# Optimization experiments

Hardware: AMD Instinct MI355X
Metric: run time of the kernel (lower is better)

## Reference

```python
import jax, jax.numpy as jnp
import numpy as np

N_NODES = 100000


def gcn_conv(x, edge_index, W, b):
    """PyG-style GCNConv: symmetric-normalized A+I propagation of x @ W, plus bias."""
    n = x.shape[0]
    src, dst = edge_index[0], edge_index[1]
    loops = jnp.arange(n, dtype=src.dtype)
    src = jnp.concatenate([src, loops])  # add self loops
    dst = jnp.concatenate([dst, loops])
    deg = jax.ops.segment_sum(jnp.ones_like(src, dtype=x.dtype), dst, num_segments=n)
    dinv = jnp.where(deg > 0, jax.lax.rsqrt(deg), 0.0)
    norm = dinv[src] * dinv[dst]  # [E+n]
    h = x @ W  # [n, out]
    msg = h[src] * norm[:, None]  # gather + scale
    out = jax.ops.segment_sum(msg, dst, num_segments=n)  # scatter-add
    return out + b


def setup_inputs() -> dict:
    key = jax.random.key(0)
    ks = jax.random.split(key, 5)
    x = jax.random.normal(ks[0], (N_NODES, 4), dtype=jnp.float32)
    edge_index = jax.random.randint(ks[1], (2, 3200000), 0, N_NODES, dtype=jnp.int64)
    W1 = jax.random.normal(ks[2], (4, 64), dtype=jnp.float32) * 0.5
    b1 = jnp.zeros((64,), dtype=jnp.float32)
    W2 = jax.random.normal(ks[3], (64, 32), dtype=jnp.float32) * 0.125
    b2 = jnp.zeros((32,), dtype=jnp.float32)
    return {"x": x, "edge_index": edge_index, "W1": W1, "b1": b1, "W2": W2, "b2": b2}


def reference(x, edge_index, W1, b1, W2, b2):
    h = gcn_conv(x, edge_index, W1, b1)
    h = jax.nn.relu(h)
    # F.dropout with training=False is identity (eval-mode reference)
    h = gcn_conv(h, edge_index, W2, b2)
    return jnp.mean(h, axis=0)  # [32]
```

## Files before the change

kernel.cpp:

```cpp
#include <hip/hip_runtime.h>

#define ST 1024
#define EPB 8192
#define HT 1024
#define FT 1024
#define S_LOG 8
#define S 256
#define CAP 8912
#define MAXB 512
#define FXS 8388608.0f
#define FXI 1.1920929e-7f

__device__ __forceinline__ void gAtomAdd(float* p, float v) {
    unsafeAtomicAdd(p, v);
}

__global__ void __launch_bounds__(ST) k_sctr2(
        const int4* __restrict__ src4, const int4* __restrict__ dst4, int E,
        int* __restrict__ cur_d, int* __restrict__ cur_s,
        unsigned* __restrict__ rec_d, unsigned* __restrict__ rec_s, int nb) {
    __shared__ unsigned lrec[EPB];
    __shared__ unsigned short lbkt[EPB];
    __shared__ int cnt[MAXB];
    __shared__ int lst[MAXB];
    __shared__ int gb[MAXB];
    __shared__ int wsum[8];
    int t = threadIdx.x;
    int lane = t & 63, wv = t >> 6;
    int E4 = E >> 2;
    int b4 = blockIdx.x * (EPB / 4);
    int m = min(EPB, E - blockIdx.x * EPB);

    int4 dk[2], sk[2];
    bool v[2];
    #pragma unroll
    for (int k = 0; k < 2; ++k) {
        int idx = b4 + k * ST + t;
        v[k] = idx < E4;
        if (v[k]) { dk[k] = dst4[idx]; sk[k] = src4[idx]; }
    }

    for (int ph = 0; ph < 2; ++ph) {
        int* cursor = ph ? cur_s : cur_d;
        unsigned* rec = ph ? rec_s : rec_d;
        if (t < MAXB) cnt[t] = 0;
        __syncthreads();
        int rk[8];
        #pragma unroll
        for (int k = 0; k < 2; ++k) {
            if (v[k]) {
                int4 K = ph ? sk[k] : dk[k];
                rk[4 * k + 0] = atomicAdd(&cnt[K.x >> S_LOG], 1);
                rk[4 * k + 1] = atomicAdd(&cnt[K.y >> S_LOG], 1);
                rk[4 * k + 2] = atomicAdd(&cnt[K.z >> S_LOG], 1);
                rk[4 * k + 3] = atomicAdd(&cnt[K.w >> S_LOG], 1);
            }
        }
        __syncthreads();
        int c = 0, ic = 0;
        if (t < MAXB) {
            c = cnt[t]; ic = c;
            #pragma unroll
            for (int o = 1; o < 64; o <<= 1) {
                int u = __shfl_up(ic, o);
                if (lane >= o) ic += u;
            }
            if (lane == 63) wsum[wv] = ic;
        }
        __syncthreads();
        if (t < MAXB) {
            int pre = 0;
            #pragma unroll
            for (int k = 0; k < 7; ++k) pre += (k < wv) ? wsum[k] : 0;
            ic += pre;
            lst[t] = ic - c;
            gb[t] = (c > 0) ? t * CAP + atomicAdd(&cursor[t], c) : 0;
        }
        __syncthreads();
        #pragma unroll
        for (int k = 0; k < 2; ++k) {
            if (v[k]) {
                int4 K = ph ? sk[k] : dk[k];
                int4 P = ph ? dk[k] : sk[k];
                int bb, p;
                bb = K.x >> S_LOG; p = lst[bb] + rk[4 * k + 0];
                lrec[p] = ((unsigned)P.x << S_LOG) | (unsigned)(K.x & (S - 1));
                lbkt[p] = (unsigned short)bb;
                bb = K.y >> S_LOG; p = lst[bb] + rk[4 * k + 1];
                lrec[p] = ((unsigned)P.y << S_LOG) | (unsigned)(K.y & (S - 1));
                lbkt[p] = (unsigned short)bb;
                bb = K.z >> S_LOG; p = lst[bb] + rk[4 * k + 2];
                lrec[p] = ((unsigned)P.z << S_LOG) | (unsigned)(K.z & (S - 1));
                lbkt[p] = (unsigned short)bb;
                bb = K.w >> S_LOG; p = lst[bb] + rk[4 * k + 3];
                lrec[p] = ((unsigned)P.w << S_LOG) | (unsigned)(K.w & (S - 1));
                lbkt[p] = (unsigned short)bb;
            }
        }
        __syncthreads();
        for (int i = t; i < m; i += ST) {
            int bb = lbkt[i];
            rec[gb[bb] + (i - lst[bb])] = lrec[i];
        }
        __syncthreads();
    }
}

__global__ void __launch_bounds__(HT) k_hist(
        const unsigned* __restrict__ rec_d, const int* __restrict__ cur_d,
        const float4* __restrict__ x, float* __restrict__ dinv,
        float4* __restrict__ y, unsigned short* __restrict__ rank16,
        int* __restrict__ degb, int n) {
    __shared__ int cnt[S];
    int b = blockIdx.x, t = threadIdx.x;
    if (t < S) cnt[t] = 0;
    __syncthreads();
    int lo = b * CAP;
    int m = cur_d[b];
    int m4 = m >> 2;
    const uint4* rec4 = (const uint4*)(rec_d + lo);
    ushort4* rk4 = (ushort4*)(rank16 + lo);
    for (int i = t; i < m4; i += HT) {
        uint4 r = rec4[i];
        int r0 = atomicAdd(&cnt[r.x & (S - 1)], 1);
        int r1 = atomicAdd(&cnt[r.y & (S - 1)], 1);
        int r2 = atomicAdd(&cnt[r.z & (S - 1)], 1);
        int r3 = atomicAdd(&cnt[r.w & (S - 1)], 1);
        rk4[i] = make_ushort4((unsigned short)r0, (unsigned short)r1,
                              (unsigned short)r2, (unsigned short)r3);
    }
    for (int i = (m4 << 2) + t; i < m; i += HT) {
        int r = atomicAdd(&cnt[rec_d[lo + i] & (S - 1)], 1);
        rank16[lo + i] = (unsigned short)r;
    }
    __syncthreads();
    if (t < S) {
        degb[(b << S_LOG) + t] = cnt[t];
        int nd = (b << S_LOG) + t;
        if (nd < n) {
            float dv = rsqrtf((float)cnt[t] + 1.0f);
            dinv[nd] = dv;
            float4 xi = x[nd];
            y[nd] = make_float4(dv * xi.x, dv * xi.y, dv * xi.z, dv * xi.w);
        }
    }
}

__global__ void __launch_bounds__(FT) k_fuse(
        const unsigned* __restrict__ rec_d, const unsigned* __restrict__ rec_s,
        const int* __restrict__ cur_d, const int* __restrict__ cur_s,
        const unsigned short* __restrict__ rank16, const int* __restrict__ degb,
        const float4* __restrict__ y, const float* __restrict__ dinv,
        const float* __restrict__ W1, const float* __restrict__ b1,
        float* __restrict__ g, int n) {
    __shared__ unsigned lrec[CAP];
    __shared__ int cnt[S];
    __shared__ int nst[S];
    __shared__ int ia[S];
    __shared__ float4 lp1[S];
    __shared__ float red[FT];
    __shared__ int wsum[4];
    int b = blockIdx.x, t = threadIdx.x;
    int lane = t & 63, wv = t >> 6;
    if (t < S) ia[t] = 0;
    int lo = b * CAP;
    int md = cur_d[b];
    int ms = cur_s[b];
    int c = 0, ic = 0;
    if (t < S) {
        c = degb[(b << S_LOG) + t]; ic = c;
        #pragma unroll
        for (int o = 1; o < 64; o <<= 1) {
            int u = __shfl_up(ic, o);
            if (lane >= o) ic += u;
        }
        if (lane == 63) wsum[wv] = ic;
    }
    __syncthreads();
    if (t < S) {
        int pre = 0;
        #pragma unroll
        for (int k = 0; k < 3; ++k) pre += (k < wv) ? wsum[k] : 0;
        ic += pre;
        cnt[t] = ic;
        nst[t] = ic - c;
    }
    __syncthreads();
    int md4 = md >> 2;
    const uint4* rd4 = (const uint4*)(rec_d + lo);
    const ushort4* rk4 = (const ushort4*)(rank16 + lo);
    for (int i = t; i < md4; i += FT) {
        uint4 r = rd4[i];
        ushort4 rk = rk4[i];
        lrec[nst[r.x & (S - 1)] + rk.x] = r.x >> S_LOG;
        lrec[nst[r.y & (S - 1)] + rk.y] = r.y >> S_LOG;
        lrec[nst[r.z & (S - 1)] + rk.z] = r.z >> S_LOG;
        lrec[nst[r.w & (S - 1)] + rk.w] = r.w >> S_LOG;
    }
    for (int i = (md4 << 2) + t; i < md; i += FT) {
        unsigned r = rec_d[lo + i];
        lrec[nst[r & (S - 1)] + rank16[lo + i]] = r >> S_LOG;
    }
    int ms4 = ms >> 2;
    const uint4* rs4 = (const uint4*)(rec_s + lo);
    for (int i = t; i < ms4; i += FT) {
        uint4 r = rs4[i];
        int d0 = (int)(dinv[r.x >> S_LOG] * FXS + 0.5f);
        int d1 = (int)(dinv[r.y >> S_LOG] * FXS + 0.5f);
        int d2 = (int)(dinv[r.z >> S_LOG] * FXS + 0.5f);
        int d3 = (int)(dinv[r.w >> S_LOG] * FXS + 0.5f);
        atomicAdd(&ia[r.x & (S - 1)], d0);
        atomicAdd(&ia[r.y & (S - 1)], d1);
        atomicAdd(&ia[r.z & (S - 1)], d2);
        atomicAdd(&ia[r.w & (S - 1)], d3);
    }
    for (int i = (ms4 << 2) + t; i < ms; i += FT) {
        unsigned r = rec_s[lo + i];
        atomicAdd(&ia[r & (S - 1)], (int)(dinv[r >> S_LOG] * FXS + 0.5f));
    }
    __syncthreads();
    int node = t >> 2, q = t & 3;
    int nd = (b << S_LOG) + node;
    if (nd < n) {
        int j1 = cnt[node];
        int j = nst[node] + q;
        float a0 = 0.0f, a1 = 0.0f, a2 = 0.0f, a3 = 0.0f;
        for (; j + 12 < j1; j += 16) {
            int s0 = lrec[j], s1 = lrec[j + 4], s2 = lrec[j + 8], s3 = lrec[j + 12];
            float4 y0 = y[s0], y1 = y[s1], y2 = y[s2], y3 = y[s3];
            a0 += y0.x + y1.x + y2.x + y3.x;
            a1 += y0.y + y1.y + y2.y + y3.y;
            a2 += y0.z + y1.z + y2.z + y3.z;
            a3 += y0.w + y1.w + y2.w + y3.w;
        }
        for (; j < j1; j += 4) {
            float4 ys = y[lrec[j]];
            a0 += ys.x; a1 += ys.y; a2 += ys.z; a3 += ys.w;
        }
        a0 += __shfl_down(a0, 2); a1 += __shfl_down(a1, 2);
        a2 += __shfl_down(a2, 2); a3 += __shfl_down(a3, 2);
        a0 += __shfl_down(a0, 1); a1 += __shfl_down(a1, 1);
        a2 += __shfl_down(a2, 1); a3 += __shfl_down(a3, 1);
        if (q == 0) {
            float di = dinv[nd];
            lp1[node] = make_float4(di * a0, di * a1, di * a2, di * a3);
        }
    }
    __syncthreads();
    int cch = t & 63, w = t >> 6;
    float w0 = W1[cch], w1 = W1[64 + cch], w2 = W1[128 + cch], w3 = W1[192 + cch];
    float bb = b1[cch];
    int nb0 = b << S_LOG;
    float facc = 0.0f;
    for (int k = w; k < S; k += 16) {
        int ndk = nb0 + k;
        if (ndk >= n) break;
        float di = dinv[ndk];
        float4 p = lp1[k];
        float4 yi = y[ndk];
        float h0 = fmaf(di, yi.x, p.x);
        float h1 = fmaf(di, yi.y, p.y);
        float h2 = fmaf(di, yi.z, p.z);
        float h3 = fmaf(di, yi.w, p.w);
        float h = fmaf(h0, w0, fmaf(h1, w1, fmaf(h2, w2, fmaf(h3, w3, bb))));
        h = fmaxf(h, 0.0f);
        float ak = (float)ia[k] * FXI;
        float wi = fmaf(di, ak, di * di);
        facc = fmaf(wi, h, facc);
    }
    red[t] = facc;
    __syncthreads();
    if (t < 64) {
        float s = red[t];
        #pragma unroll
        for (int o = 1; o < 16; ++o) s += red[t + 64 * o];
        gAtomAdd(&g[t], s);
    }
}

__global__ void k_final(const float* __restrict__ g, const float* __restrict__ W2,
                        const float* __restrict__ b2, float* __restrict__ out, float inv_n) {
    int j = threadIdx.x;
    if (j < 32) {
        float a = 0.0f;
        #pragma unroll
        for (int c = 0; c < 64; ++c) a = fmaf(g[c], W2[c * 32 + j], a);
        out[j] = fmaf(a, inv_n, b2[j]);
    }
}

extern "C" void kernel_launch(void* const* d_in, const int* in_sizes, int n_in,
                              void* d_out, int out_size, void* d_ws, size_t ws_size,
                              hipStream_t stream) {
    const float* x  = (const float*)d_in[0];
    const int*   ei = (const int*)d_in[1];
    const float* W1 = (const float*)d_in[2];
    const float* b1 = (const float*)d_in[3];
    const float* W2 = (const float*)d_in[4];
    const float* b2 = (const float*)d_in[5];
    float* out = (float*)d_out;

    int n = in_sizes[0] / 4;
    int E = in_sizes[1] / 2;
    const int* src = ei;
    const int* dst = ei + E;
    int NB = (n + S - 1) >> S_LOG;

    char* ws = (char*)d_ws;
    int* cur_d = (int*)ws;
    int* cur_s = cur_d + 512;
    float* g   = (float*)(cur_s + 512);
    size_t ctrl = 1600;
    unsigned* rec_d = (unsigned*)ws + ctrl;
    unsigned* rec_s = rec_d + (size_t)NB * CAP;
    float* y    = (float*)(rec_s + (size_t)NB * CAP);
    float* dinv = y + 4 * (size_t)n;
    int* degb   = (int*)(dinv + (size_t)n);
    unsigned short* rank16 = (unsigned short*)(degb + (size_t)NB * 256);

    int NSB = (E + EPB - 1) / EPB;

    hipMemsetAsync(ws, 0, ctrl * 4, stream);
    k_sctr2<<<NSB, ST, 0, stream>>>((const int4*)src, (const int4*)dst, E,
                                    cur_d, cur_s, rec_d, rec_s, NB);
    k_hist<<<NB, HT, 0, stream>>>(rec_d, cur_d, (const float4*)x, dinv,
                                  (float4*)y, rank16, degb, n);
    k_fuse<<<NB, FT, 0, stream>>>(rec_d, rec_s, cur_d, cur_s, rank16, degb,
                                  (const float4*)y, dinv, W1, b1, g, n);
    k_final<<<1, 64, 0, stream>>>(g, W2, b2, out, 1.0f / (float)n);
}
```

Baseline: 146.0 us.

## Split scatter phases and overlap source scatter with degree histogram

The two-phase scatter kernel is split. Destination bucketing runs alone in k_sctr_d. A new combined kernel runs the source-bucketing blocks and the per-bucket degree histogram/rank blocks in a single launch, so these independent stages overlap on the GPU instead of running serially. The cost is that k_sctr_d and k_combo each load src and dst again, adding one extra pass over the edge index. k_combo also carries the larger LDS footprint from the scatter path, which can lower occupancy for the histogram blocks.

```diff
diff --git a/kernel.cpp b/kernel.cpp
--- a/kernel.cpp
+++ b/kernel.cpp
@@ -2,7 +2,6 @@
 
 #define ST 1024
 #define EPB 8192
-#define HT 1024
 #define FT 1024
 #define S_LOG 8
 #define S 256
@@ -15,16 +14,15 @@
     unsafeAtomicAdd(p, v);
 }
 
-__global__ void __launch_bounds__(ST) k_sctr2(
+__global__ void __launch_bounds__(ST) k_sctr_d(
         const int4* __restrict__ src4, const int4* __restrict__ dst4, int E,
-        int* __restrict__ cur_d, int* __restrict__ cur_s,
-        unsigned* __restrict__ rec_d, unsigned* __restrict__ rec_s, int nb) {
+        int* __restrict__ cur_d, unsigned* __restrict__ rec_d) {
     __shared__ unsigned lrec[EPB];
     __shared__ unsigned short lbkt[EPB];
     __shared__ int cnt[MAXB];
     __shared__ int lst[MAXB];
     __shared__ int gb[MAXB];
-    __shared__ int wsum[8];
+    __shared__ int wsum[16];
     int t = threadIdx.x;
     int lane = t & 63, wv = t >> 6;
     int E4 = E >> 2;
@@ -39,21 +37,103 @@
         v[k] = idx < E4;
         if (v[k]) { dk[k] = dst4[idx]; sk[k] = src4[idx]; }
     }
-
-    for (int ph = 0; ph < 2; ++ph) {
-        int* cursor = ph ? cur_s : cur_d;
-        unsigned* rec = ph ? rec_s : rec_d;
+    if (t < MAXB) cnt[t] = 0;
+    __syncthreads();
+    int rk[8];
+    #pragma unroll
+    for (int k = 0; k < 2; ++k) {
+        if (v[k]) {
+            rk[4 * k + 0] = atomicAdd(&cnt[dk[k].x >> S_LOG], 1);
+            rk[4 * k + 1] = atomicAdd(&cnt[dk[k].y >> S_LOG], 1);
+            rk[4 * k + 2] = atomicAdd(&cnt[dk[k].z >> S_LOG], 1);
+            rk[4 * k + 3] = atomicAdd(&cnt[dk[k].w >> S_LOG], 1);
+        }
+    }
+    __syncthreads();
+    int c = 0, ic = 0;
+    if (t < MAXB) {
+        c = cnt[t]; ic = c;
+        #pragma unroll
+        for (int o = 1; o < 64; o <<= 1) {
+            int u = __shfl_up(ic, o);
+            if (lane >= o) ic += u;
+        }
+        if (lane == 63) wsum[wv] = ic;
+    }
+    __syncthreads();
+    if (t < MAXB) {
+        int pre = 0;
+        #pragma unroll
+        for (int k = 0; k < 7; ++k) pre += (k < wv) ? wsum[k] : 0;
+        ic += pre;
+        lst[t] = ic - c;
+        gb[t] = (c > 0) ? t * CAP + atomicAdd(&cur_d[t], c) : 0;
+    }
+    __syncthreads();
+    #pragma unroll
+    for (int k = 0; k < 2; ++k) {
+        if (v[k]) {
+            int4 K = dk[k]; int4 P = sk[k];
+            int bb, p;
+            bb = K.x >> S_LOG; p = lst[bb] + rk[4 * k + 0];
+            lrec[p] = ((unsigned)P.x << S_LOG) | (unsigned)(K.x & (S - 1));
+            lbkt[p] = (unsigned short)bb;
+            bb = K.y >> S_LOG; p = lst[bb] + rk[4 * k + 1];
+            lrec[p] = ((unsigned)P.y << S_LOG) | (unsigned)(K.y & (S - 1));
+            lbkt[p] = (unsigned short)bb;
+            bb = K.z >> S_LOG; p = lst[bb] + rk[4 * k + 2];
+            lrec[p] = ((unsigned)P.z << S_LOG) | (unsigned)(K.z & (S - 1));
+            lbkt[p] = (unsigned short)bb;
+            bb = K.w >> S_LOG; p = lst[bb] + rk[4 * k + 3];
+            lrec[p] = ((unsigned)P.w << S_LOG) | (unsigned)(K.w & (S - 1));
+            lbkt[p] = (unsigned short)bb;
+        }
+    }
+    __syncthreads();
+    for (int i = t; i < m; i += ST) {
+        int bb = lbkt[i];
+        rec_d[gb[bb] + (i - lst[bb])] = lrec[i];
+    }
+}
+
+__global__ void __launch_bounds__(ST) k_combo(
+        const int4* __restrict__ src4, const int4* __restrict__ dst4, int E,
+        int* __restrict__ cur_s, unsigned* __restrict__ rec_s,
+        const unsigned* __restrict__ rec_d, const int* __restrict__ cur_d,
+        const float4* __restrict__ x, float* __restrict__ dinv,
+        float4* __restrict__ y, unsigned short* __restrict__ rank16,
+        int* __restrict__ degb, int n, int NSB) {
+    __shared__ unsigned lrec[EPB];
+    __shared__ unsigned short lbkt[EPB];
+    __shared__ int cnt[MAXB];
+    __shared__ int lst[MAXB];
+    __shared__ int gb[MAXB];
+    __shared__ int wsum[16];
+    int t = threadIdx.x;
+    int lane = t & 63, wv = t >> 6;
+
+    if (blockIdx.x < NSB) {
+        int E4 = E >> 2;
+        int b4 = blockIdx.x * (EPB / 4);
+        int m = min(EPB, E - blockIdx.x * EPB);
+        int4 dk[2], sk[2];
+        bool v[2];
+        #pragma unroll
+        for (int k = 0; k < 2; ++k) {
+            int idx = b4 + k * ST + t;
+            v[k] = idx < E4;
+            if (v[k]) { dk[k] = dst4[idx]; sk[k] = src4[idx]; }
+        }
         if (t < MAXB) cnt[t] = 0;
         __syncthreads();
         int rk[8];
         #pragma unroll
         for (int k = 0; k < 2; ++k) {
             if (v[k]) {
-                int4 K = ph ? sk[k] : dk[k];
-                rk[4 * k + 0] = atomicAdd(&cnt[K.x >> S_LOG], 1);
-                rk[4 * k + 1] = atomicAdd(&cnt[K.y >> S_LOG], 1);
-                rk[4 * k + 2] = atomicAdd(&cnt[K.z >> S_LOG], 1);
-                rk[4 * k + 3] = atomicAdd(&cnt[K.w >> S_LOG], 1);
+                rk[4 * k + 0] = atomicAdd(&cnt[sk[k].x >> S_LOG], 1);
+                rk[4 * k + 1] = atomicAdd(&cnt[sk[k].y >> S_LOG], 1);
+                rk[4 * k + 2] = atomicAdd(&cnt[sk[k].z >> S_LOG], 1);
+                rk[4 * k + 3] = atomicAdd(&cnt[sk[k].w >> S_LOG], 1);
             }
         }
         __syncthreads();
@@ -74,14 +154,13 @@
             for (int k = 0; k < 7; ++k) pre += (k < wv) ? wsum[k] : 0;
             ic += pre;
             lst[t] = ic - c;
-            gb[t] = (c > 0) ? t * CAP + atomicAdd(&cursor[t], c) : 0;
+            gb[t] = (c > 0) ? t * CAP + atomicAdd(&cur_s[t], c) : 0;
         }
         __syncthreads();
         #pragma unroll
         for (int k = 0; k < 2; ++k) {
             if (v[k]) {
-                int4 K = ph ? sk[k] : dk[k];
-                int4 P = ph ? dk[k] : sk[k];
+                int4 K = sk[k]; int4 P = dk[k];
                 int bb, p;
                 bb = K.x >> S_LOG; p = lst[bb] + rk[4 * k + 0];
                 lrec[p] = ((unsigned)P.x << S_LOG) | (unsigned)(K.x & (S - 1));
@@ -100,48 +179,40 @@
         __syncthreads();
         for (int i = t; i < m; i += ST) {
             int bb = lbkt[i];
-            rec[gb[bb] + (i - lst[bb])] = lrec[i];
-        }
-        __syncthreads();
-    }
-}
-
-__global__ void __launch_bounds__(HT) k_hist(
-        const unsigned* __restrict__ rec_d, const int* __restrict__ cur_d,
-        const float4* __restrict__ x, float* __restrict__ dinv,
-        float4* __restrict__ y, unsigned short* __restrict__ rank16,
-        int* __restrict__ degb, int n) {
-    __shared__ int cnt[S];
-    int b = blockIdx.x, t = threadIdx.x;
-    if (t < S) cnt[t] = 0;
-    __syncthreads();
-    int lo = b * CAP;
-    int m = cur_d[b];
-    int m4 = m >> 2;
-    const uint4* rec4 = (const uint4*)(rec_d + lo);
-    ushort4* rk4 = (ushort4*)(rank16 + lo);
-    for (int i = t; i < m4; i += HT) {
-        uint4 r = rec4[i];
-        int r0 = atomicAdd(&cnt[r.x & (S - 1)], 1);
-        int r1 = atomicAdd(&cnt[r.y & (S - 1)], 1);
-        int r2 = atomicAdd(&cnt[r.z & (S - 1)], 1);
-        int r3 = atomicAdd(&cnt[r.w & (S - 1)], 1);
-        rk4[i] = make_ushort4((unsigned short)r0, (unsigned short)r1,
-                              (unsigned short)r2, (unsigned short)r3);
-    }
-    for (int i = (m4 << 2) + t; i < m; i += HT) {
-        int r = atomicAdd(&cnt[rec_d[lo + i] & (S - 1)], 1);
-        rank16[lo + i] = (unsigned short)r;
-    }
-    __syncthreads();
-    if (t < S) {
-        degb[(b << S_LOG) + t] = cnt[t];
-        int nd = (b << S_LOG) + t;
-        if (nd < n) {
-            float dv = rsqrtf((float)cnt[t] + 1.0f);
-            dinv[nd] = dv;
-            float4 xi = x[nd];
-            y[nd] = make_float4(dv * xi.x, dv * xi.y, dv * xi.z, dv * xi.w);
+            rec_s[gb[bb] + (i - lst[bb])] = lrec[i];
+        }
+    } else {
+        int b = blockIdx.x - NSB;
+        if (t < S) cnt[t] = 0;
+        __syncthreads();
+        int lo = b * CAP;
+        int m = cur_d[b];
+        int m4 = m >> 2;
+        const uint4* rec4 = (const uint4*)(rec_d + lo);
+        ushort4* rk4 = (ushort4*)(rank16 + lo);
+        for (int i = t; i < m4; i += ST) {
+            uint4 r = rec4[i];
+            int r0 = atomicAdd(&cnt[r.x & (S - 1)], 1);
+            int r1 = atomicAdd(&cnt[r.y & (S - 1)], 1);
+            int r2 = atomicAdd(&cnt[r.z & (S - 1)], 1);
+            int r3 = atomicAdd(&cnt[r.w & (S - 1)], 1);
+            rk4[i] = make_ushort4((unsigned short)r0, (unsigned short)r1,
+                                  (unsigned short)r2, (unsigned short)r3);
+        }
+        for (int i = (m4 << 2) + t; i < m; i += ST) {
+            int r = atomicAdd(&cnt[rec_d[lo + i] & (S - 1)], 1);
+            rank16[lo + i] = (unsigned short)r;
+        }
+        __syncthreads();
+        if (t < S) {
+            degb[(b << S_LOG) + t] = cnt[t];
+            int nd = (b << S_LOG) + t;
+            if (nd < n) {
+                float dv = rsqrtf((float)cnt[t] + 1.0f);
+                dinv[nd] = dv;
+                float4 xi = x[nd];
+                y[nd] = make_float4(dv * xi.x, dv * xi.y, dv * xi.z, dv * xi.w);
+            }
         }
     }
 }
@@ -321,10 +392,12 @@
     int NSB = (E + EPB - 1) / EPB;
 
     hipMemsetAsync(ws, 0, ctrl * 4, stream);
-    k_sctr2<<<NSB, ST, 0, stream>>>((const int4*)src, (const int4*)dst, E,
-                                    cur_d, cur_s, rec_d, rec_s, NB);
-    k_hist<<<NB, HT, 0, stream>>>(rec_d, cur_d, (const float4*)x, dinv,
-                                  (float4*)y, rank16, degb, n);
+    k_sctr_d<<<NSB, ST, 0, stream>>>((const int4*)src, (const int4*)dst, E,
+                                     cur_d, rec_d);
+    k_combo<<<NSB + NB, ST, 0, stream>>>((const int4*)src, (const int4*)dst, E,
+                                         cur_s, rec_s, rec_d, cur_d,
+                                         (const float4*)x, dinv, (float4*)y,
+                                         rank16, degb, n, NSB);
     k_fuse<<<NB, FT, 0, stream>>>(rec_d, rec_s, cur_d, cur_s, rank16, degb,
                                   (const float4*)y, dinv, W1, b1, g, n);
     k_final<<<1, 64, 0, stream>>>(g, W2, b2, out, 1.0f / (float)n);
```

After: 155.1 us. 1.06x slower.
